# Kernel tuning notes

Hardware: AMD Instinct MI355X
Metric: run time of the kernel (lower is better)

The kernel has to match this reference:

```python
import jax, jax.numpy as jnp
import numpy as np

P, N, F, H, D_HID = 3, 4096, 1024, 8, 8
EMBED = H * D_HID  # 64
ATT, C = 128, 16


def setup_inputs() -> dict:
    key = jax.random.key(0)
    ks = jax.random.split(key, 12)
    return {
        "inputs": jax.random.normal(ks[0], (P, N, F), jnp.float32),
        # bias_mat plays the role of an additive adjacency mask; random floats are fine for math checking
        "bias_mat": jax.random.normal(ks[1], (P, N, N), jnp.float32),
        "W": jax.random.normal(ks[2], (P, H, F, D_HID), jnp.float32) * 0.05,
        "a1_w": jax.random.normal(ks[3], (P, H, D_HID), jnp.float32) * 0.1,
        "a1_b": jax.random.normal(ks[4], (P, H), jnp.float32) * 0.1,
        "a2_w": jax.random.normal(ks[5], (P, H, D_HID), jnp.float32) * 0.1,
        "a2_b": jax.random.normal(ks[6], (P, H), jnp.float32) * 0.1,
        "h_bias": jnp.zeros((P, H, D_HID), jnp.float32),
        "Ws": jax.random.normal(ks[7], (EMBED, ATT), jnp.float32) * 0.1,
        "bs": jax.random.normal(ks[8], (ATT,), jnp.float32) * 0.1,
        "u": jax.random.normal(ks[9], (ATT,), jnp.float32) * 0.1,
        "Wc": jax.random.normal(ks[10], (EMBED, C), jnp.float32) * 0.05,
        "bc": jnp.zeros((C,), jnp.float32),
    }


def reference(inputs, bias_mat, W, a1_w, a1_b, a2_w, a2_b, h_bias, Ws, bs, u, Wc, bc):
    # inputs: [P,N,F], bias_mat: [P,N,N]
    embeds = []
    for p in range(inputs.shape[0]):  # small fixed loop over meta-paths
        seq = inputs[p]                                            # [N,F]
        fts = jnp.einsum('nf,hfd->hnd', seq, W[p])                 # shared projection, all heads
        f1 = jnp.einsum('hnd,hd->hn', fts, a1_w[p]) + a1_b[p][:, None]
        f2 = jnp.einsum('hnd,hd->hn', fts, a2_w[p]) + a2_b[p][:, None]
        logits = f1[:, :, None] + f2[:, None, :]                   # [H,N,N] additive attention
        coefs = jax.nn.softmax(jax.nn.leaky_relu(logits) + bias_mat[p][None], axis=-1)
        vals = jnp.einsum('hnm,hmd->hnd', coefs, fts) + h_bias[p][:, None, :]
        h = jax.nn.elu(vals)                                       # activation per head
        embeds.append(jnp.transpose(h, (1, 0, 2)).reshape(h.shape[1], -1))  # concat heads -> [N,H*d]
    multi = jnp.stack(embeds, axis=1)                              # [N,P,EMBED]
    # semantic (meta-path) attention
    v = jnp.tanh(multi @ Ws + bs)                                  # [N,P,ATT]
    alphas = jax.nn.softmax(v @ u, axis=-1)                        # [N,P]
    final = jnp.sum(multi * alphas[:, :, None], axis=1)            # [N,EMBED]
    # single final classifier head (mean over 1 head == identity)
    logits_out = final @ Wc + bc                                   # [N,C]
    return logits_out, final, alphas
```

## Files before the change

kernel.cpp:

```cpp
#include <hip/hip_runtime.h>

#define LOG2E 1.44269504088896f

typedef _Float16 f16;
typedef _Float16 f16x8 __attribute__((ext_vector_type(8)));
typedef float f32x4 __attribute__((ext_vector_type(4)));

#define NP 3
#define NN 4096
#define FF 1024
#define HH 8
#define DD 8
#define HD 64

#define OFF_F1S   0
#define OFF_F2S   393216
#define OFF_F2MAX 589824
#define OFF_FTST  590080
#define OFF_MULTI 2162944

#define OUT_FINAL 65536
#define OUT_ALPHA 327680

__global__ __launch_bounds__(256) void kA(const float* __restrict__ inp,
                                          const float* __restrict__ W,
                                          const float* __restrict__ a1w,
                                          const float* __restrict__ a1b,
                                          const float* __restrict__ a2w,
                                          const float* __restrict__ a2b,
                                          char* __restrict__ ws) {
    __shared__ float At[32 * 68];
    __shared__ float Bt[32 * 64];
    __shared__ float ftile[64 * 68];
    const int tid = threadIdx.x;
    const int p = blockIdx.y;
    const int n0 = blockIdx.x * 64;

    const int tr = tid >> 4, tc = tid & 15;
    const int r0 = tr * 4, c0 = tc * 4;
    const int sr = tid >> 2, sq = tid & 3;
    const int bc = tid & 63, bkq = tid >> 6;
    const int hB = bc >> 3, dB = bc & 7;

    float acc[4][4] = {};

    for (int kb = 0; kb < 32; ++kb) {
        const float* asrc = inp + ((size_t)p * NN + n0 + sr) * FF + kb * 32 + sq * 8;
        float4 v0 = *(const float4*)asrc;
        float4 v1 = *(const float4*)(asrc + 4);
        int kbase = sq * 8;
        At[(kbase + 0) * 68 + sr] = v0.x; At[(kbase + 1) * 68 + sr] = v0.y;
        At[(kbase + 2) * 68 + sr] = v0.z; At[(kbase + 3) * 68 + sr] = v0.w;
        At[(kbase + 4) * 68 + sr] = v1.x; At[(kbase + 5) * 68 + sr] = v1.y;
        At[(kbase + 6) * 68 + sr] = v1.z; At[(kbase + 7) * 68 + sr] = v1.w;
        #pragma unroll
        for (int i = 0; i < 8; ++i) {
            int k = bkq * 8 + i;
            Bt[k * 64 + bc] = W[(((size_t)p * HH + hB) * FF + kb * 32 + k) * DD + dB];
        }
        __syncthreads();
        #pragma unroll
        for (int k = 0; k < 32; ++k) {
            float4 av = *(const float4*)&At[k * 68 + r0];
            float4 bv = *(const float4*)&Bt[k * 64 + c0];
            float aa[4] = {av.x, av.y, av.z, av.w};
            float bb[4] = {bv.x, bv.y, bv.z, bv.w};
            #pragma unroll
            for (int i = 0; i < 4; ++i)
                #pragma unroll
                for (int j = 0; j < 4; ++j) acc[i][j] += aa[i] * bb[j];
        }
        __syncthreads();
    }
    #pragma unroll
    for (int i = 0; i < 4; ++i) {
        float4 o;
        o.x = acc[i][0]; o.y = acc[i][1]; o.z = acc[i][2]; o.w = acc[i][3];
        *(float4*)&ftile[(r0 + i) * 68 + c0] = o;
    }
    __syncthreads();

    float* f1s = (float*)(ws + OFF_F1S);
    f16* f2s = (f16*)(ws + OFF_F2S);
    #pragma unroll
    for (int rep = 0; rep < 2; ++rep) {
        int task = tid + rep * 256;
        int row = task >> 3, h = task & 7;
        const float* fb = &ftile[row * 68 + h * 8];
        float s1 = a1b[p * HH + h], s2 = a2b[p * HH + h];
        #pragma unroll
        for (int d = 0; d < 8; ++d) {
            float v = fb[d];
            s1 += v * a1w[((size_t)p * HH + h) * DD + d];
            s2 += v * a2w[((size_t)p * HH + h) * DD + d];
        }
        f1s[((size_t)p * HH + h) * NN + n0 + row] = s1 * LOG2E;
        f2s[((size_t)p * HH + h) * NN + n0 + row] = (f16)(s2 * LOG2E);
    }
    {
        f16* ftsT = (f16*)(ws + OFF_FTST);
        int cc2 = tid >> 2, rq = (tid & 3) * 16;
        union { f16 h[16]; uint4 u[2]; } pk;
        #pragma unroll
        for (int i = 0; i < 16; ++i) pk.h[i] = (f16)ftile[(rq + i) * 68 + cc2];
        uint4* dst = (uint4*)(ftsT + ((size_t)p * HD + cc2) * NN + n0 + rq);
        dst[0] = pk.u[0];
        dst[1] = pk.u[1];
    }
}

__global__ __launch_bounds__(64) void kA2(char* __restrict__ ws) {
    const f16* f2s = (const f16*)(ws + OFF_F2S);
    float* fmax = (float*)(ws + OFF_F2MAX);
    int b = blockIdx.x;
    int lane = threadIdx.x;
    float v = -1e30f;
    for (int m = lane; m < NN; m += 64) v = fmaxf(v, (float)f2s[(size_t)b * NN + m]);
    #pragma unroll
    for (int off = 32; off >= 1; off >>= 1) v = fmaxf(v, __shfl_xor(v, off, 64));
    if (lane == 0) fmax[b] = v;
}

__global__ __launch_bounds__(256) void kB(const float* __restrict__ bias,
                                          const float* __restrict__ h_bias,
                                          char* __restrict__ ws) {
    __shared__ __align__(16) char smem[42768];
    f16* ftsL = (f16*)smem;
    float* f2L = (float*)(smem + 34320);

    const int tid = threadIdx.x;
    const int lane = tid & 63, wv = tid >> 6;
    const int c = lane & 15, kg = lane >> 4;
    const int p = blockIdx.y;
    const int n0 = blockIdx.x * 16;
    const int n = n0 + c;

    const float* f1s = (const float*)(ws + OFF_F1S);
    const f16* f2s = (const f16*)(ws + OFF_F2S);
    const float* fmax = (const float*)(ws + OFF_F2MAX);
    const f16* ftsG = (const f16*)(ws + OFF_FTST);
    float* multi = (float*)(ws + OFF_MULTI);

    float A1[8], B1[8];
    #pragma unroll
    for (int h = 0; h < 8; ++h) {
        float f1v = f1s[((size_t)p * 8 + h) * NN + n];
        float fm = fmax[p * 8 + h];
        float x = f1v + fm;
        float lr = fmaxf(x, 0.01f * x);
        float ub = lr + 8.0f * LOG2E;
        A1[h] = f1v - ub;
        B1[h] = fmaf(0.01f, f1v, -ub);
    }

    for (int i = tid; i < 264; i += 256) ftsL[64 * 264 + i] = (f16)1.0f;

    const int sg = tid >> 3, se = tid & 7;
    const int srow = sg & 7, sq = sg >> 3;
    const int f2r = tid >> 5, f2c = (tid & 31) * 8;

    const f16* ftsP = ftsG + (size_t)p * HD * NN;
    const f16* f2P = f2s + (size_t)p * 8 * NN;

    const int rowsel = (c < 8) ? c * 264 : 64 * 264;
    const int hstep = (c < 8) ? 8 * 264 : 0;

    const float* bb_base = bias + ((size_t)p * NN + n) * NN + wv * 64 + kg * 8;

    f32x4 acc[8] = {};

    float4 uA0 = *(const float4*)(bb_base);
    float4 uA1 = *(const float4*)(bb_base + 4);
    float4 uB0 = *(const float4*)(bb_base + 32);
    float4 uB1 = *(const float4*)(bb_base + 36);

    #pragma unroll 1
    for (int ch = 0; ch < 16; ++ch) {
        const int m0 = ch * 256;
        const int chn = (ch + 1 < 16) ? ch + 1 : 15;
        const float* bpn = bb_base + chn * 256;
        float4 nA0 = *(const float4*)(bpn);
        float4 nA1 = *(const float4*)(bpn + 4);
        float4 nB0 = *(const float4*)(bpn + 32);
        float4 nB1 = *(const float4*)(bpn + 36);

        {
            const f16* gsrc = ftsP + m0 + sq * 64 + se * 8;
            f16* ldst = ftsL + srow * 264 + sq * 64 + se * 8;
            #pragma unroll
            for (int k = 0; k < 8; ++k) {
                *(uint4*)(ldst + k * 8 * 264) =
                    *(const uint4*)(gsrc + (size_t)(srow + k * 8) * NN);
            }
        }
        {
            union { uint4 u; f16 h[8]; } t16;
            t16.u = *(const uint4*)(f2P + (size_t)f2r * NN + m0 + f2c);
            float4 lo, hi;
            lo.x = (float)t16.h[0]; lo.y = (float)t16.h[1];
            lo.z = (float)t16.h[2]; lo.w = (float)t16.h[3];
            hi.x = (float)t16.h[4]; hi.y = (float)t16.h[5];
            hi.z = (float)t16.h[6]; hi.w = (float)t16.h[7];
            *(float4*)(f2L + f2r * 264 + f2c) = lo;
            *(float4*)(f2L + f2r * 264 + f2c + 4) = hi;
        }
        __syncthreads();

        #pragma unroll
        for (int s = 0; s < 2; ++s) {
            const int mloc = wv * 64 + s * 32 + kg * 8;
            float4 bv0 = s ? uB0 : uA0;
            float4 bv1 = s ? uB1 : uA1;
            float bbl[8] = {bv0.x * LOG2E, bv0.y * LOG2E, bv0.z * LOG2E, bv0.w * LOG2E,
                            bv1.x * LOG2E, bv1.y * LOG2E, bv1.z * LOG2E, bv1.w * LOG2E};
            #pragma unroll
            for (int h = 0; h < 8; ++h) {
                const float* f2p = f2L + h * 264 + mloc;
                float4 f2a = *(const float4*)f2p;
                float4 f2b = *(const float4*)(f2p + 4);
                float f2arr[8] = {f2a.x, f2a.y, f2a.z, f2a.w, f2b.x, f2b.y, f2b.z, f2b.w};
                f16x8 bf = *(const f16x8*)(ftsL + rowsel + h * hstep + mloc);
                union { f16x8 v; f16 e[8]; } af;
                #pragma unroll
                for (int j = 0; j < 8; ++j) {
                    float t1 = f2arr[j] + A1[h];
                    float t2 = fmaf(0.01f, f2arr[j], B1[h]);
                    af.e[j] = (f16)__builtin_amdgcn_exp2f(fmaxf(t1, t2) + bbl[j]);
                }
                acc[h] = __builtin_amdgcn_mfma_f32_16x16x32_f16(af.v, bf, acc[h], 0, 0, 0);
            }
        }
        __syncthreads();
        uA0 = nA0; uA1 = nA1; uB0 = nB0; uB1 = nB1;
    }

    float* red = (float*)smem;
    #pragma unroll
    for (int h = 0; h < 8; ++h) {
        if (c <= 8) {
            #pragma unroll
            for (int r = 0; r < 4; ++r)
                red[((wv * 8 + h) * 16 + kg * 4 + r) * 9 + c] = acc[h][r];
        }
    }
    __syncthreads();
    #pragma unroll
    for (int rep = 0; rep < 4; ++rep) {
        int idx = tid + rep * 256;
        int R = idx >> 6, hd = idx & 63;
        int h = hd >> 3, d = hd & 7;
        float v = 0.f, l = 0.f;
        #pragma unroll
        for (int w = 0; w < 4; ++w) {
            v += red[((w * 8 + h) * 16 + R) * 9 + d];
            l += red[((w * 8 + h) * 16 + R) * 9 + 8];
        }
        float o = v / l + h_bias[(p * 8 + h) * 8 + d];
        o = o > 0.f ? o : (__builtin_amdgcn_exp2f(o * LOG2E) - 1.0f);
        multi[((size_t)(n0 + R) * NP + p) * HD + hd] = o;
    }
}

__global__ __launch_bounds__(256) void kC(const float* __restrict__ Ws,
                                          const float* __restrict__ bsv,
                                          const float* __restrict__ uv,
                                          const float* __restrict__ Wc,
                                          const float* __restrict__ bcv,
                                          char* __restrict__ ws,
                                          float* __restrict__ out) {
    __shared__ float WsL[64 * 128];
    __shared__ float mult[16 * 3 * 64];
    __shared__ float WcL[64 * 16];
    __shared__ float uL[128], bsL[128], bcL[16];
    __shared__ float vred[16 * 3 * 16];
    __shared__ float alphaL[16 * 3];
    __shared__ float fin[16 * 64];
    const int tid = threadIdx.x;
    const int n0 = blockIdx.x * 16;
    const float* multi = (const float*)(ws + OFF_MULTI);

    for (int i = tid; i < 64 * 128; i += 256) WsL[i] = Ws[i];
    for (int i = tid; i < 3072; i += 256) mult[i] = multi[(size_t)n0 * 192 + i];
    for (int i = tid; i < 1024; i += 256) WcL[i] = Wc[i];
    if (tid < 128) { uL[tid] = uv[tid]; bsL[tid] = bsv[tid]; }
    if (tid < 16) bcL[tid] = bcv[tid];
    __syncthreads();

    const int nl = tid >> 4, j = tid & 15;
    for (int p = 0; p < 3; ++p) {
        float va[8] = {};
        for (int e = 0; e < 64; ++e) {
            float me = mult[(nl * 3 + p) * 64 + e];
            #pragma unroll
            for (int i = 0; i < 8; ++i) va[i] += me * WsL[e * 128 + j + 16 * i];
        }
        float part = 0.f;
        #pragma unroll
        for (int i = 0; i < 8; ++i) part += tanhf(va[i] + bsL[j + 16 * i]) * uL[j + 16 * i];
        vred[(nl * 3 + p) * 16 + j] = part;
    }
    __syncthreads();
    if (tid < 16) {
        float sc[3];
        for (int p = 0; p < 3; ++p) {
            float s = 0.f;
            for (int jj = 0; jj < 16; ++jj) s += vred[(tid * 3 + p) * 16 + jj];
            sc[p] = s;
        }
        float mx = fmaxf(sc[0], fmaxf(sc[1], sc[2]));
        float e0 = __builtin_amdgcn_exp2f((sc[0] - mx) * LOG2E);
        float e1 = __builtin_amdgcn_exp2f((sc[1] - mx) * LOG2E);
        float e2 = __builtin_amdgcn_exp2f((sc[2] - mx) * LOG2E);
        float inv = 1.f / (e0 + e1 + e2);
        float a0 = e0 * inv, a1 = e1 * inv, a2 = e2 * inv;
        alphaL[tid * 3 + 0] = a0; alphaL[tid * 3 + 1] = a1; alphaL[tid * 3 + 2] = a2;
        out[OUT_ALPHA + (size_t)(n0 + tid) * 3 + 0] = a0;
        out[OUT_ALPHA + (size_t)(n0 + tid) * 3 + 1] = a1;
        out[OUT_ALPHA + (size_t)(n0 + tid) * 3 + 2] = a2;
    }
    __syncthreads();
    for (int idx = tid; idx < 1024; idx += 256) {
        int nn2 = idx >> 6, e = idx & 63;
        float f = 0.f;
        for (int p = 0; p < 3; ++p) f += mult[(nn2 * 3 + p) * 64 + e] * alphaL[nn2 * 3 + p];
        fin[nn2 * 64 + e] = f;
        out[OUT_FINAL + (size_t)(n0 + nn2) * 64 + e] = f;
    }
    __syncthreads();
    {
        int nn2 = tid >> 4, cc2 = tid & 15;
        float lg = bcL[cc2];
        for (int e = 0; e < 64; ++e) lg += fin[nn2 * 64 + e] * WcL[e * 16 + cc2];
        out[(size_t)(n0 + nn2) * 16 + cc2] = lg;
    }
}

extern "C" void kernel_launch(void* const* d_in, const int* in_sizes, int n_in,
                              void* d_out, int out_size, void* d_ws, size_t ws_size,
                              hipStream_t stream) {
    (void)in_sizes; (void)n_in; (void)out_size; (void)ws_size;
    const float* inp = (const float*)d_in[0];
    const float* bias = (const float*)d_in[1];
    const float* W = (const float*)d_in[2];
    const float* a1w = (const float*)d_in[3];
    const float* a1b = (const float*)d_in[4];
    const float* a2w = (const float*)d_in[5];
    const float* a2b = (const float*)d_in[6];
    const float* hb = (const float*)d_in[7];
    const float* Wsv = (const float*)d_in[8];
    const float* bsv = (const float*)d_in[9];
    const float* uv = (const float*)d_in[10];
    const float* Wcv = (const float*)d_in[11];
    const float* bcv = (const float*)d_in[12];
    char* ws = (char*)d_ws;
    float* out = (float*)d_out;

    hipLaunchKernelGGL(kA, dim3(64, 3), dim3(256), 0, stream, inp, W, a1w, a1b, a2w, a2b, ws);
    hipLaunchKernelGGL(kA2, dim3(24), dim3(64), 0, stream, ws);
    hipLaunchKernelGGL(kB, dim3(256, 3), dim3(256), 0, stream, bias, hb, ws);
    hipLaunchKernelGGL(kC, dim3(256), dim3(256), 0, stream, Wsv, bsv, uv, Wcv, bcv, ws, out);
}
```

Measured before the change: 467.9 us.

## Halve kA row tile for more blocks and register-prefetch kB tiles

```diff
diff --git a/kernel.cpp b/kernel.cpp
--- a/kernel.cpp
+++ b/kernel.cpp
@@ -29,30 +29,28 @@
                                           const float* __restrict__ a2w,
                                           const float* __restrict__ a2b,
                                           char* __restrict__ ws) {
-    __shared__ float At[32 * 68];
+    __shared__ float At[32 * 36];
     __shared__ float Bt[32 * 64];
-    __shared__ float ftile[64 * 68];
+    __shared__ float ftile[32 * 68];
     const int tid = threadIdx.x;
     const int p = blockIdx.y;
-    const int n0 = blockIdx.x * 64;
+    const int n0 = blockIdx.x * 32;
 
     const int tr = tid >> 4, tc = tid & 15;
-    const int r0 = tr * 4, c0 = tc * 4;
-    const int sr = tid >> 2, sq = tid & 3;
+    const int r0 = tr * 2, c0 = tc * 4;
+    const int sr = tid >> 3, sak = (tid & 7) * 4;
     const int bc = tid & 63, bkq = tid >> 6;
     const int hB = bc >> 3, dB = bc & 7;
 
-    float acc[4][4] = {};
+    float acc[2][4] = {};
 
     for (int kb = 0; kb < 32; ++kb) {
-        const float* asrc = inp + ((size_t)p * NN + n0 + sr) * FF + kb * 32 + sq * 8;
-        float4 v0 = *(const float4*)asrc;
-        float4 v1 = *(const float4*)(asrc + 4);
-        int kbase = sq * 8;
-        At[(kbase + 0) * 68 + sr] = v0.x; At[(kbase + 1) * 68 + sr] = v0.y;
-        At[(kbase + 2) * 68 + sr] = v0.z; At[(kbase + 3) * 68 + sr] = v0.w;
-        At[(kbase + 4) * 68 + sr] = v1.x; At[(kbase + 5) * 68 + sr] = v1.y;
-        At[(kbase + 6) * 68 + sr] = v1.z; At[(kbase + 7) * 68 + sr] = v1.w;
+        const float* asrc = inp + ((size_t)p * NN + n0 + sr) * FF + kb * 32 + sak;
+        float4 av = *(const float4*)asrc;
+        At[(sak + 0) * 36 + sr] = av.x;
+        At[(sak + 1) * 36 + sr] = av.y;
+        At[(sak + 2) * 36 + sr] = av.z;
+        At[(sak + 3) * 36 + sr] = av.w;
         #pragma unroll
         for (int i = 0; i < 8; ++i) {
             int k = bkq * 8 + i;
@@ -61,19 +59,19 @@
         __syncthreads();
         #pragma unroll
         for (int k = 0; k < 32; ++k) {
-            float4 av = *(const float4*)&At[k * 68 + r0];
+            float2 a2 = *(const float2*)&At[k * 36 + r0];
             float4 bv = *(const float4*)&Bt[k * 64 + c0];
-            float aa[4] = {av.x, av.y, av.z, av.w};
-            float bb[4] = {bv.x, bv.y, bv.z, bv.w};
+            float bb4[4] = {bv.x, bv.y, bv.z, bv.w};
             #pragma unroll
-            for (int i = 0; i < 4; ++i)
-                #pragma unroll
-                for (int j = 0; j < 4; ++j) acc[i][j] += aa[i] * bb[j];
+            for (int j = 0; j < 4; ++j) {
+                acc[0][j] += a2.x * bb4[j];
+                acc[1][j] += a2.y * bb4[j];
+            }
         }
         __syncthreads();
     }
     #pragma unroll
-    for (int i = 0; i < 4; ++i) {
+    for (int i = 0; i < 2; ++i) {
         float4 o;
         o.x = acc[i][0]; o.y = acc[i][1]; o.z = acc[i][2]; o.w = acc[i][3];
         *(float4*)&ftile[(r0 + i) * 68 + c0] = o;
@@ -82,10 +80,8 @@
 
     float* f1s = (float*)(ws + OFF_F1S);
     f16* f2s = (f16*)(ws + OFF_F2S);
-    #pragma unroll
-    for (int rep = 0; rep < 2; ++rep) {
-        int task = tid + rep * 256;
-        int row = task >> 3, h = task & 7;
+    {
+        int row = tid >> 3, h = tid & 7;
         const float* fb = &ftile[row * 68 + h * 8];
         float s1 = a1b[p * HH + h], s2 = a2b[p * HH + h];
         #pragma unroll
@@ -99,13 +95,11 @@
     }
     {
         f16* ftsT = (f16*)(ws + OFF_FTST);
-        int cc2 = tid >> 2, rq = (tid & 3) * 16;
-        union { f16 h[16]; uint4 u[2]; } pk;
-        #pragma unroll
-        for (int i = 0; i < 16; ++i) pk.h[i] = (f16)ftile[(rq + i) * 68 + cc2];
-        uint4* dst = (uint4*)(ftsT + ((size_t)p * HD + cc2) * NN + n0 + rq);
-        dst[0] = pk.u[0];
-        dst[1] = pk.u[1];
+        int cc2 = tid >> 2, rq = (tid & 3) * 8;
+        union { f16 h[8]; uint4 u; } pk;
+        #pragma unroll
+        for (int i = 0; i < 8; ++i) pk.h[i] = (f16)ftile[(rq + i) * 68 + cc2];
+        *(uint4*)(ftsT + ((size_t)p * HD + cc2) * NN + n0 + rq) = pk.u;
     }
 }
 
@@ -169,42 +163,48 @@
 
     f32x4 acc[8] = {};
 
+    uint4 rf[8];
+    uint4 rf2v;
+
+    auto issue = [&](int ch) {
+        const f16* gsrc = ftsP + ch * 256 + sq * 64 + se * 8;
+        #pragma unroll
+        for (int k = 0; k < 8; ++k)
+            rf[k] = *(const uint4*)(gsrc + (size_t)(srow + k * 8) * NN);
+        rf2v = *(const uint4*)(f2P + (size_t)f2r * NN + ch * 256 + f2c);
+    };
+    auto commit = [&]() {
+        f16* ldst = ftsL + srow * 264 + sq * 64 + se * 8;
+        #pragma unroll
+        for (int k = 0; k < 8; ++k) *(uint4*)(ldst + k * 8 * 264) = rf[k];
+        union { uint4 u; f16 h[8]; } t16;
+        t16.u = rf2v;
+        float4 lo, hi;
+        lo.x = (float)t16.h[0]; lo.y = (float)t16.h[1];
+        lo.z = (float)t16.h[2]; lo.w = (float)t16.h[3];
+        hi.x = (float)t16.h[4]; hi.y = (float)t16.h[5];
+        hi.z = (float)t16.h[6]; hi.w = (float)t16.h[7];
+        *(float4*)(f2L + f2r * 264 + f2c) = lo;
+        *(float4*)(f2L + f2r * 264 + f2c + 4) = hi;
+    };
+
+    issue(0);
+    commit();
+    issue(1);
     float4 uA0 = *(const float4*)(bb_base);
     float4 uA1 = *(const float4*)(bb_base + 4);
     float4 uB0 = *(const float4*)(bb_base + 32);
     float4 uB1 = *(const float4*)(bb_base + 36);
+    __syncthreads();
 
     #pragma unroll 1
     for (int ch = 0; ch < 16; ++ch) {
-        const int m0 = ch * 256;
         const int chn = (ch + 1 < 16) ? ch + 1 : 15;
         const float* bpn = bb_base + chn * 256;
         float4 nA0 = *(const float4*)(bpn);
         float4 nA1 = *(const float4*)(bpn + 4);
         float4 nB0 = *(const float4*)(bpn + 32);
         float4 nB1 = *(const float4*)(bpn + 36);
-
-        {
-            const f16* gsrc = ftsP + m0 + sq * 64 + se * 8;
-            f16* ldst = ftsL + srow * 264 + sq * 64 + se * 8;
-            #pragma unroll
-            for (int k = 0; k < 8; ++k) {
-                *(uint4*)(ldst + k * 8 * 264) =
-                    *(const uint4*)(gsrc + (size_t)(srow + k * 8) * NN);
-            }
-        }
-        {
-            union { uint4 u; f16 h[8]; } t16;
-            t16.u = *(const uint4*)(f2P + (size_t)f2r * NN + m0 + f2c);
-            float4 lo, hi;
-            lo.x = (float)t16.h[0]; lo.y = (float)t16.h[1];
-            lo.z = (float)t16.h[2]; lo.w = (float)t16.h[3];
-            hi.x = (float)t16.h[4]; hi.y = (float)t16.h[5];
-            hi.z = (float)t16.h[6]; hi.w = (float)t16.h[7];
-            *(float4*)(f2L + f2r * 264 + f2c) = lo;
-            *(float4*)(f2L + f2r * 264 + f2c + 4) = hi;
-        }
-        __syncthreads();
 
         #pragma unroll
         for (int s = 0; s < 2; ++s) {
@@ -231,6 +231,11 @@
             }
         }
         __syncthreads();
+        if (ch < 15) {
+            commit();
+            if (ch < 14) issue(ch + 2);
+            __syncthreads();
+        }
         uA0 = nA0; uA1 = nA1; uB0 = nB0; uB1 = nB1;
     }
 
@@ -355,7 +360,7 @@
     char* ws = (char*)d_ws;
     float* out = (float*)d_out;
 
-    hipLaunchKernelGGL(kA, dim3(64, 3), dim3(256), 0, stream, inp, W, a1w, a1b, a2w, a2b, ws);
+    hipLaunchKernelGGL(kA, dim3(128, 3), dim3(256), 0, stream, inp, W, a1w, a1b, a2w, a2b, ws);
     hipLaunchKernelGGL(kA2, dim3(24), dim3(64), 0, stream, ws);
     hipLaunchKernelGGL(kB, dim3(256, 3), dim3(256), 0, stream, bias, hb, ws);
     hipLaunchKernelGGL(kC, dim3(256), dim3(256), 0, stream, Wsv, bsv, uv, Wcv, bcv, ws, out);
```

After: 516.8 us. 10.5% more time.
